# Kernel optimization log

Measured on AMD Instinct MI355X. Metric: run time of the kernel, lower is better.

The kernel has to match this reference:

```python
import jax, jax.numpy as jnp
import numpy as np

ALPHA = 0.2   # LeakyReLU negative slope (init arg alpha)
H = 256       # hidden_dim
U = 1024      # user pairs -> 2U user nodes
M = 64        # UAV nodes
D = 2 * U     # uniform out-degree per UAV (edges sorted by source)
N = 2 * U + M
E = M * D


def _lstm_dir(x, w_ih, w_hh, b):
    # x: [T, B, I] -> outputs [T, B, Hc]; b = b_ih + b_hh (they only ever add)
    Hc = w_hh.shape[1]
    B = x.shape[1]
    def step(carry, xt):
        h, c = carry
        g = xt @ w_ih.T + h @ w_hh.T + b          # [B, 4*Hc], gate order i,f,g,o
        i, f, gg, o = jnp.split(g, 4, axis=-1)
        c = jax.nn.sigmoid(f) * c + jax.nn.sigmoid(i) * jnp.tanh(gg)
        h = jax.nn.sigmoid(o) * jnp.tanh(c)
        return (h, c), h
    h0 = jnp.zeros((B, Hc), x.dtype)
    _, hs = jax.lax.scan(step, (h0, h0), x)
    return hs


def _bilstm(x, wih, whh, b):
    # wih: [2, 4Hc, I]; whh: [2, 4Hc, Hc]; b: [2, 4Hc]; dir 0 = fwd, 1 = reverse
    fwd = _lstm_dir(x, wih[0], whh[0], b[0])
    rev = _lstm_dir(x[::-1], wih[1], whh[1], b[1])[::-1]
    return jnp.concatenate([fwd, rev], axis=-1)   # [T, B, 2*Hc]


def _mlp2(h, w1, b1, w2, b2):
    h = jax.nn.relu(h @ w1.T + b1)
    return jax.nn.relu(h @ w2.T + b2)


def _forward(x, edge_index, users_num,
             ul_wih, ul_whh, ul_b, uav_lin_w, uav_lin_b,
             msg_w1, msg_b1, msg_w2, msg_b2,
             wq_w, wq_b, wr_w, wr_b, att_w, att_b,
             upd_w1, upd_b1, upd_w2, upd_b2,
             uavl_wih, uavl_whh, uavl_b, lin2_w, lin2_b):
    Un = users_num
    n = x.shape[0]
    m = n - 2 * Un
    # ---- users bidirectional LSTM over the pair (seq_len=2, batch=U) ----
    seq = jnp.stack([x[:Un], x[Un:2 * Un]], axis=0)        # [2, U, 2]
    users = _bilstm(seq, ul_wih, ul_whh, ul_b)             # [2, U, H]
    users = jnp.concatenate([users[0], users[1]], axis=0)  # [2U, H]
    uavs = x[2 * Un:] @ uav_lin_w.T + uav_lin_b            # [M, H]
    h = jnp.concatenate([users, uavs], axis=0)             # [N, H]
    # ---- message passing (flow target_to_source: i=src, aggregate at src) ----
    src, tgt = edge_index[0], edge_index[1]
    xi = h[src]                                            # [E, H]
    xj = h[tgt]                                            # [E, H]
    msg = _mlp2(jnp.concatenate([xi, xj], axis=1), msg_w1, msg_b1, msg_w2, msg_b2)  # [E, H]
    q = xi @ wq_w.T + wq_b
    r = msg @ wr_w.T + wr_b
    a = jax.nn.leaky_relu(jnp.concatenate([q, r], axis=1) @ att_w.T + att_b, ALPHA)  # [E,1]
    # segment softmax: edges sorted by source, uniform degree -> reshape [M, D]
    a = jax.nn.softmax(a.reshape(m, -1), axis=1).reshape(-1, 1)
    # ---- scatter-mean aggregate over source index ----
    agg = jax.ops.segment_sum(a * msg, src, num_segments=n)          # [N, H]
    cnt = jax.ops.segment_sum(jnp.ones((src.shape[0],), x.dtype), src, num_segments=n)
    agg = agg / jnp.maximum(cnt, 1.0)[:, None]
    # ---- update ----
    h2 = _mlp2(jnp.concatenate([agg, h], axis=1), upd_w1, upd_b1, upd_w2, upd_b2)  # [N, H]
    uav_seq = h2[2 * Un:][:, None, :]                      # [M, 1, H]
    uav_out = _bilstm(uav_seq, uavl_wih, uavl_whh, uavl_b)[:, 0, :]  # [M, H]
    out = jnp.concatenate([h2[:2 * Un], uav_out], axis=0)
    return jax.nn.sigmoid(out @ lin2_w.T + lin2_b)         # [N, 2]


def setup_inputs():
    key = jax.random.key(0)
    ks = iter(jax.random.split(key, 32))
    p = lambda *s: jax.random.normal(next(ks), s, jnp.float32) * 0.05
    Hc = H // 2
    x = jax.random.uniform(next(ks), (N, 2), jnp.float32)
    src = jnp.repeat(2 * U + jnp.arange(M), D)
    tgt = jnp.tile(jnp.arange(2 * U), M)
    edge_index = jnp.stack([src, tgt]).astype(jnp.int32)
    return dict(
        x=x, edge_index=edge_index, users_num=U,
        ul_wih=p(2, 4 * Hc, 2), ul_whh=p(2, 4 * Hc, Hc), ul_b=p(2, 4 * Hc),
        uav_lin_w=p(H, 2), uav_lin_b=p(H),
        msg_w1=p(H, 2 * H), msg_b1=p(H), msg_w2=p(H, H), msg_b2=p(H),
        wq_w=p(H, H), wq_b=p(H), wr_w=p(H, H), wr_b=p(H),
        att_w=p(1, 2 * H), att_b=p(1),
        upd_w1=p(H, 2 * H), upd_b1=p(H), upd_w2=p(H, H), upd_b2=p(H),
        uavl_wih=p(2, 4 * Hc, H), uavl_whh=p(2, 4 * Hc, Hc), uavl_b=p(2, 4 * Hc),
        lin2_w=p(2, H), lin2_b=p(2),
    )


def reference(x, edge_index, users_num,
              ul_wih, ul_whh, ul_b, uav_lin_w, uav_lin_b,
              msg_w1, msg_b1, msg_w2, msg_b2,
              wq_w, wq_b, wr_w, wr_b, att_w, att_b,
              upd_w1, upd_b1, upd_w2, upd_b2,
              uavl_wih, uavl_whh, uavl_b, lin2_w, lin2_b):
    return _forward(x, edge_index, users_num,
                    ul_wih, ul_whh, ul_b, uav_lin_w, uav_lin_b,
                    msg_w1, msg_b1, msg_w2, msg_b2,
                    wq_w, wq_b, wr_w, wr_b, att_w, att_b,
                    upd_w1, upd_b1, upd_w2, upd_b2,
                    uavl_wih, uavl_whh, uavl_b, lin2_w, lin2_b)
```

## Files before the change

kernel.cpp:

```cpp
#include <hip/hip_runtime.h>
#include <hip/hip_bf16.h>
#include <math.h>

#define UQ   1024
#define NUQ  2048
#define MQ   64
#define NN   2112
#define HD   256

typedef __attribute__((ext_vector_type(4))) float f32x4;
typedef __attribute__((ext_vector_type(8))) __bf16 bf16x8;

#define OFF_HB    0u
#define OFF_HUF   65536u
#define OFF_ACATF 1146880u
#define OFF_PUBF  3309568u
#define OFF_PB    4358144u
#define OFF_SPR   4423680u
#define OFF_ATT   4423936u
#define OFF_WHHT  4426240u
#define OFF_WIHT  4950528u
#define OFF_W1F   5999104u
#define OFF_W2F   6261248u
#define OFF_UW1F  6392320u
#define OFF_UW2F  6654464u
#define OFF_L1BF  6785536u
#define OFF_CREC  7866880u
#define OFF_H2    8399360u

__device__ __forceinline__ float sigm(float v) { return 1.f / (1.f + expf(-v)); }

__device__ __forceinline__ int huf_idx(int row, int k) {
  return (((row >> 6) * 8 + (k >> 5)) * 4 + ((row >> 4) & 3)) * 512 +
         (((k >> 3) & 3) * 16 + (row & 15)) * 8 + (k & 7);
}
__device__ __forceinline__ int acatf_idx(int row, int k) {
  return (((row >> 6) * 16 + (k >> 5)) * 4 + ((row >> 4) & 3)) * 512 +
         (((k >> 3) & 3) * 16 + (row & 15)) * 8 + (k & 7);
}
__device__ __forceinline__ int pubf_idx(int row, int k) {
  return (((row >> 8) * 8 + (k >> 5)) * 16 + ((row >> 4) & 15)) * 512 +
         (((k >> 3) & 3) * 16 + (row & 15)) * 8 + (k & 7);
}

__device__ __forceinline__ void gl16(const void* g, void* l) {
  __builtin_amdgcn_global_load_lds((const __attribute__((address_space(1))) void*)g,
                                   (__attribute__((address_space(3))) void*)l, 16, 0, 0);
}

__device__ void tile_transpose_perm(const float* __restrict__ in, int in_ld,
                                    float* __restrict__ out, int out_ld,
                                    int k0, int c0) {
  __shared__ float ldt[64][68];
  const int t = threadIdx.x;
  {
    const int ci = t >> 2, kq = t & 3;
    const int c = c0 + ci;
    const int row = (c & 3) * 128 + (c >> 2);
    const float* src = in + row * in_ld + k0 + kq * 16;
#pragma unroll
    for (int e = 0; e < 4; ++e)
      *(f32x4*)&ldt[ci][kq * 16 + e * 4] = *(const f32x4*)(src + e * 4);
  }
  __syncthreads();
  {
    const int kk = t >> 2, cq = t & 3;
    float* dst = out + (k0 + kk) * out_ld + c0 + cq * 16;
#pragma unroll
    for (int e4 = 0; e4 < 4; ++e4) {
      f32x4 v;
#pragma unroll
      for (int j = 0; j < 4; ++j) v[j] = ldt[cq * 16 + e4 * 4 + j][kk];
      *(f32x4*)(dst + e4 * 4) = v;
    }
  }
}

template<int K>
__device__ void frag_cast16(const float* __restrict__ W, int j0, __bf16* __restrict__ frag) {
  __shared__ float ldc[16][K + 4];
  const int t = threadIdx.x;
  {
    const int jr = t >> 4, kq = t & 15;
    const float* src = W + (j0 + jr) * K + kq * (K / 16);
#pragma unroll
    for (int e = 0; e < K / 64; ++e)
      *(f32x4*)&ldc[jr][kq * (K / 16) + e * 4] = *(const f32x4*)(src + e * 4);
  }
  __syncthreads();
  const int f = j0 >> 4;
  constexpr int nks = K >> 5;
  constexpr int thr_per_ks = 256 / nks;
  constexpr int q_per_thr = 512 / thr_per_ks;
  const int ks = t / thr_per_ks;
  const int q0 = (t % thr_per_ks) * q_per_thr;
#pragma unroll
  for (int h = 0; h < q_per_thr / 8; ++h) {
    bf16x8 v;
#pragma unroll
    for (int e = 0; e < 8; ++e) {
      int q = q0 + h * 8 + e;
      int lane = q >> 3;
      v[e] = (__bf16)ldc[lane & 15][ks * 32 + (lane >> 4) * 8 + (q & 7)];
    }
    *(bf16x8*)(frag + (ks * 16 + f) * 512 + q0 + h * 8) = v;
  }
}

__global__ __launch_bounds__(256) void k0_prep(
    const float* __restrict__ ul_whh, const float* __restrict__ uavl_wih,
    const float* __restrict__ msg_w1, const float* __restrict__ msg_w2,
    const float* __restrict__ upd_w1, const float* __restrict__ upd_w2,
    const float* __restrict__ att_w,  const float* __restrict__ att_b,
    const float* __restrict__ wq_w,   const float* __restrict__ wq_b,
    const float* __restrict__ wr_w,   const float* __restrict__ wr_b,
    char* __restrict__ ws)
{
  const int b = blockIdx.x, t = threadIdx.x;
  if (b < 32) {
    const int dir = b >> 4, tile = b & 15;
    tile_transpose_perm(ul_whh + dir * 65536, 128,
                        (float*)(ws + OFF_WHHT) + dir * 65536, 512,
                        (tile >> 3) * 64, (tile & 7) * 64);
  } else if (b < 96) {
    const int b2 = b - 32, dir = b2 >> 5, tile = b2 & 31;
    tile_transpose_perm(uavl_wih + dir * 131072, 256,
                        (float*)(ws + OFF_WIHT) + dir * 131072, 512,
                        (tile >> 3) * 64, (tile & 7) * 64);
  } else if (b < 112) {
    frag_cast16<256>(msg_w2, (b - 96) * 16, (__bf16*)(ws + OFF_W2F));
  } else if (b < 128) {
    frag_cast16<512>(msg_w1, (b - 112) * 16, (__bf16*)(ws + OFF_W1F));
  } else if (b < 144) {
    frag_cast16<512>(upd_w1, (b - 128) * 16, (__bf16*)(ws + OFF_UW1F));
  } else if (b < 160) {
    frag_cast16<256>(upd_w2, (b - 144) * 16, (__bf16*)(ws + OFF_UW2F));
  } else {
    float* wqa = (float*)(ws + OFF_ATT);
    float* vv  = wqa + 256;
    float* c0  = wqa + 512;
    float sa = 0.f, sr = 0.f;
    for (int j = 0; j < 256; ++j) {
      sa += att_w[j]       * wq_w[j * 256 + t];
      sr += att_w[256 + j] * wr_w[j * 256 + t];
    }
    wqa[t] = sa; vv[t] = sr;
    __shared__ float red[256];
    red[t] = att_w[t] * wq_b[t] + att_w[256 + t] * wr_b[t];
    __syncthreads();
    for (int s = 128; s > 0; s >>= 1) { if (t < s) red[t] += red[t + s]; __syncthreads(); }
    if (t == 0) c0[0] = red[0] + att_b[0];
  }
}

__global__ __launch_bounds__(256) void k1_embed(
    const float* __restrict__ x, const float* __restrict__ ul_wih,
    const float* __restrict__ ul_b, const float* __restrict__ uav_lin_w,
    const float* __restrict__ uav_lin_b, char* __restrict__ ws)
{
  __bf16* huf   = (__bf16*)(ws + OFF_HUF);
  __bf16* acatf = (__bf16*)(ws + OFF_ACATF);
  const int b = blockIdx.x, tid = threadIdx.x;
  if (b < 256) {
    const float* whhT = (const float*)(ws + OFF_WHHT);
    const int dir = tid >> 7, hc = tid & 127;
    const int u0 = b * 4;
    float wx[4], wy[4], bb[4];
#pragma unroll
    for (int g = 0; g < 4; ++g) {
      int row = g * 128 + hc;
      wx[g] = ul_wih[dir * 1024 + row * 2 + 0];
      wy[g] = ul_wih[dir * 1024 + row * 2 + 1];
      bb[g] = ul_b[dir * 512 + row];
    }
    __shared__ float h1s[2][128][4];
    float c1[4], h1v[4], in1x[4], in1y[4];
#pragma unroll
    for (int uu = 0; uu < 4; ++uu) {
      int u = u0 + uu;
      float ax = x[u * 2], ay = x[u * 2 + 1];
      float bx = x[(UQ + u) * 2], by = x[(UQ + u) * 2 + 1];
      float i0x = dir ? bx : ax, i0y = dir ? by : ay;
      in1x[uu] = dir ? ax : bx; in1y[uu] = dir ? ay : by;
      float gv[4];
#pragma unroll
      for (int g = 0; g < 4; ++g) gv[g] = wx[g] * i0x + wy[g] * i0y + bb[g];
      float ii = sigm(gv[0]), gg = tanhf(gv[2]), oo = sigm(gv[3]);
      c1[uu] = ii * gg;
      h1v[uu] = oo * tanhf(c1[uu]);
      h1s[dir][hc][uu] = h1v[uu];
    }
    __syncthreads();
    float acc[4][4];
#pragma unroll
    for (int uu = 0; uu < 4; ++uu)
#pragma unroll
      for (int g = 0; g < 4; ++g) acc[uu][g] = wx[g] * in1x[uu] + wy[g] * in1y[uu] + bb[g];
    for (int k = 0; k < 128; ++k) {
      f32x4 hv  = *(const f32x4*)&h1s[dir][k][0];
      f32x4 wv4 = *(const f32x4*)(whhT + dir * 65536 + k * 512 + hc * 4);
#pragma unroll
      for (int uu = 0; uu < 4; ++uu)
#pragma unroll
        for (int g = 0; g < 4; ++g) acc[uu][g] += hv[uu] * wv4[g];
    }
    const int col = dir * 128 + hc;
#pragma unroll
    for (int uu = 0; uu < 4; ++uu) {
      int u = u0 + uu;
      float ii = sigm(acc[uu][0]), ff = sigm(acc[uu][1]);
      float gg = tanhf(acc[uu][2]), oo = sigm(acc[uu][3]);
      float c2 = ff * c1[uu] + ii * gg;
      float h2v = oo * tanhf(c2);
      float va = dir ? h2v : h1v[uu];
      float vb = dir ? h1v[uu] : h2v;
      huf[huf_idx(u, col)] = (__bf16)va;
      huf[huf_idx(UQ + u, col)] = (__bf16)vb;
      acatf[acatf_idx(u, 256 + col)] = (__bf16)va;
      acatf[acatf_idx(UQ + u, 256 + col)] = (__bf16)vb;
      acatf[acatf_idx(u, tid)] = (__bf16)0.f;
      acatf[acatf_idx(UQ + u, tid)] = (__bf16)0.f;
    }
  } else {
    float* hb = (float*)(ws + OFF_HB);
    const int j = tid;
    const int mb = (b - 256) * 16;
    for (int m = mb; m < mb + 16; ++m) {
      float xa = x[(NUQ + m) * 2], xb = x[(NUQ + m) * 2 + 1];
      float val = xa * uav_lin_w[j * 2] + xb * uav_lin_w[j * 2 + 1] + uav_lin_b[j];
      hb[m * 256 + j] = val;
      huf[huf_idx(NUQ + m, j)] = (__bf16)val;
      acatf[acatf_idx(NUQ + m, 256 + j)] = (__bf16)val;
    }
  }
}

template<int NKS>
__device__ __forceinline__ void frag_gemm_acc(const __bf16* __restrict__ Abase,
                                              const __bf16* __restrict__ Bbase,
                                              f32x4 acc[4][4]) {
  const int lane = threadIdx.x & 63;
  const int cg = threadIdx.x >> 6;
  for (int ks = 0; ks < NKS; ++ks) {
    bf16x8 Af[4], Bf[4];
#pragma unroll
    for (int g = 0; g < 4; ++g)
      Af[g] = *(const bf16x8*)(Abase + ((ks * 4 + g) * 64 + lane) * 8);
#pragma unroll
    for (int f = 0; f < 4; ++f)
      Bf[f] = *(const bf16x8*)(Bbase + ((ks * 16 + cg * 4 + f) * 64 + lane) * 8);
#pragma unroll
    for (int g = 0; g < 4; ++g)
#pragma unroll
      for (int f = 0; f < 4; ++f)
        acc[g][f] = __builtin_amdgcn_mfma_f32_16x16x32_bf16(Af[g], Bf[f], acc[g][f], 0, 0, 0);
  }
}

__global__ __launch_bounds__(256) void k2_proj(const float* __restrict__ msg_b1,
                                               char* __restrict__ ws)
{
  const __bf16* huf = (const __bf16*)(ws + OFF_HUF);
  const __bf16* w1f = (const __bf16*)(ws + OFF_W1F);
  const int b = blockIdx.x;
  const int lane = threadIdx.x & 63, cg = threadIdx.x >> 6;
  const int cl = lane & 15, g16 = lane >> 4;
  if (b < 32) {
    f32x4 acc[4][4] = {};
    frag_gemm_acc<8>(huf + b * 16384, w1f + 65536, acc);
    __bf16* pubf = (__bf16*)(ws + OFF_PUBF);
#pragma unroll
    for (int g = 0; g < 4; ++g)
#pragma unroll
      for (int f = 0; f < 4; ++f)
#pragma unroll
        for (int r = 0; r < 4; ++r) {
          int row = b * 64 + g * 16 + g16 * 4 + r;
          int col = cg * 64 + f * 16 + cl;
          pubf[pubf_idx(row, col)] = (__bf16)acc[g][f][r];
        }
  } else if (b == 32) {
    f32x4 acc[4][4] = {};
    frag_gemm_acc<8>(huf + 32 * 16384, w1f, acc);
    float* pb = (float*)(ws + OFF_PB);
#pragma unroll
    for (int g = 0; g < 4; ++g)
#pragma unroll
      for (int f = 0; f < 4; ++f)
#pragma unroll
        for (int r = 0; r < 4; ++r) {
          int row = g * 16 + g16 * 4 + r;
          int col = cg * 64 + f * 16 + cl;
          pb[row * 256 + col] = acc[g][f][r] + msg_b1[col];
        }
  } else {
    const float* hb  = (const float*)(ws + OFF_HB);
    const float* wqa = (const float*)(ws + OFF_ATT);
    const float* c0  = wqa + 512;
    float* spr = (float*)(ws + OFF_SPR);
    const int t = threadIdx.x;
    if (t < 64) {
      float s = 0.f;
      for (int k = 0; k < 256; ++k) s += hb[t * 256 + k] * wqa[k];
      spr[t] = s + c0[0];
    }
  }
}

__global__ __launch_bounds__(1024) void k3_edge(const float* __restrict__ msg_b2,
                                                char* __restrict__ ws)
{
  const char*  PUBF = (const char*)(ws + OFF_PUBF);
  const float* PB   = (const float*)(ws + OFF_PB);
  const float* spr  = (const float*)(ws + OFF_SPR);
  const float* vv   = (const float*)(ws + OFF_ATT) + 256;
  const char*  W2F  = (const char*)(ws + OFF_W2F);
  float* crec = (float*)(ws + OFF_CREC);

  __shared__ __align__(16) char bufA[2][16384];
  __shared__ __align__(16) char bufB[2][16384];
  __shared__ float plds[16][64];
  __shared__ float redmax[16], wds[16];
  __shared__ float wvs[4][256];

  const int m = blockIdx.x >> 3, ch = blockIdx.x & 7;
  const int tid = threadIdx.x, wave = tid >> 6, lane = tid & 63;
  const int cl = lane & 15, g16 = lane >> 4;
  const int rg = wave >> 2, cg = wave & 3;
  const float sm = spr[m];
  const char* Asrc = PUBF + ch * 131072;

  gl16(Asrc + wave * 1024 + lane * 16, &bufA[0][wave * 1024]);
  gl16(W2F  + wave * 1024 + lane * 16, &bufB[0][wave * 1024]);
  __syncthreads();

  f32x4 acc[4][4] = {};
  for (int ks = 0; ks < 8; ++ks) {
    const int cur = ks & 1;
    if (ks < 7) {
      gl16(Asrc + (ks + 1) * 16384 + wave * 1024 + lane * 16, &bufA[cur ^ 1][wave * 1024]);
      gl16(W2F  + (ks + 1) * 16384 + wave * 1024 + lane * 16, &bufB[cur ^ 1][wave * 1024]);
    }
    const float* pbp = PB + m * 256 + ks * 32 + g16 * 8;
    f32x4 pb0 = *(const f32x4*)pbp;
    f32x4 pb1 = *(const f32x4*)(pbp + 4);
    bf16x8 Af[4];
#pragma unroll
    for (int g = 0; g < 4; ++g) {
      bf16x8 raw = *(const bf16x8*)(&bufA[cur][((rg * 4 + g) * 64 + lane) * 16]);
      bf16x8 a;
#pragma unroll
      for (int r = 0; r < 4; ++r) {
        a[r]     = (__bf16)fmaxf((float)raw[r]     + pb0[r], 0.f);
        a[4 + r] = (__bf16)fmaxf((float)raw[4 + r] + pb1[r], 0.f);
      }
      Af[g] = a;
    }
    bf16x8 Bf[4];
#pragma unroll
    for (int f = 0; f < 4; ++f)
      Bf[f] = *(const bf16x8*)(&bufB[cur][((cg * 4 + f) * 64 + lane) * 16]);
#pragma unroll
    for (int g = 0; g < 4; ++g)
#pragma unroll
      for (int f = 0; f < 4; ++f)
        acc[g][f] = __builtin_amdgcn_mfma_f32_16x16x32_bf16(Af[g], Bf[f], acc[g][f], 0, 0, 0);
    __syncthreads();
  }

  float p[4][4] = {};
#pragma unroll
  for (int f = 0; f < 4; ++f) {
    const int j = cg * 64 + f * 16 + cl;
    const float b2j = msg_b2[j], vj = vv[j];
#pragma unroll
    for (int g = 0; g < 4; ++g)
#pragma unroll
      for (int r = 0; r < 4; ++r) {
        float mv = fmaxf(acc[g][f][r] + b2j, 0.f);
        acc[g][f][r] = mv;
        p[g][r] += mv * vj;
      }
  }
#pragma unroll
  for (int mask = 1; mask < 16; mask <<= 1)
#pragma unroll
    for (int g = 0; g < 4; ++g)
#pragma unroll
      for (int r = 0; r < 4; ++r) p[g][r] += __shfl_xor(p[g][r], mask);
  if (cl == 0) {
#pragma unroll
    for (int g = 0; g < 4; ++g)
#pragma unroll
      for (int r = 0; r < 4; ++r) plds[wave][g * 16 + g16 * 4 + r] = p[g][r];
  }
  __syncthreads();

  float lr[4][4], wm = -3.4e38f;
#pragma unroll
  for (int g = 0; g < 4; ++g)
#pragma unroll
    for (int r = 0; r < 4; ++r) {
      int row = g * 16 + g16 * 4 + r;
      float l = plds[rg * 4 + 0][row] + plds[rg * 4 + 1][row] +
                plds[rg * 4 + 2][row] + plds[rg * 4 + 3][row] + sm;
      l = l > 0.f ? l : 0.2f * l;
      lr[g][r] = l;
      wm = fmaxf(wm, l);
    }
  wm = fmaxf(wm, __shfl_xor(wm, 16));
  wm = fmaxf(wm, __shfl_xor(wm, 32));
  if (lane == 0) redmax[wave] = wm;
  __syncthreads();
  float Mc = redmax[0];
#pragma unroll
  for (int i = 1; i < 16; ++i) Mc = fmaxf(Mc, redmax[i]);

  float e[4][4], ds = 0.f;
#pragma unroll
  for (int g = 0; g < 4; ++g)
#pragma unroll
    for (int r = 0; r < 4; ++r) { e[g][r] = __expf(lr[g][r] - Mc); ds += e[g][r]; }
  ds += __shfl_xor(ds, 16);
  ds += __shfl_xor(ds, 32);
  if (lane == 0) wds[wave] = ds;

#pragma unroll
  for (int f = 0; f < 4; ++f) {
    float w = 0.f;
#pragma unroll
    for (int g = 0; g < 4; ++g)
#pragma unroll
      for (int r = 0; r < 4; ++r) w += e[g][r] * acc[g][f][r];
    w += __shfl_xor(w, 16);
    w += __shfl_xor(w, 32);
    if (g16 == 0) wvs[rg][cg * 64 + f * 16 + cl] = w;
  }
  __syncthreads();

  float* rec = crec + (m * 8 + ch) * 260;
  if (tid < 256) rec[tid] = wvs[0][tid] + wvs[1][tid] + wvs[2][tid] + wvs[3][tid];
  if (tid == 0) rec[256] = Mc;
  if (tid == 1) rec[257] = wds[0] + wds[4] + wds[8] + wds[12];
}

__global__ __launch_bounds__(256) void k4_combine(char* __restrict__ ws)
{
  const float* crec = (const float*)(ws + OFF_CREC);
  __bf16* acatf = (__bf16*)(ws + OFF_ACATF);
  const int m = blockIdx.x, j = threadIdx.x;
  float mx = -3.4e38f;
  for (int c = 0; c < 8; ++c) mx = fmaxf(mx, crec[(m * 8 + c) * 260 + 256]);
  float S = 0.f, A = 0.f;
  for (int c = 0; c < 8; ++c) {
    const float* rec = crec + (m * 8 + c) * 260;
    float sc = __expf(rec[256] - mx);
    S += sc * rec[257];
    A += sc * rec[j];
  }
  float agg = A / S * (1.f / 2048.f);
  acatf[acatf_idx(NUQ + m, j)] = (__bf16)agg;
}

__global__ __launch_bounds__(256) void k5_upd1(const float* __restrict__ upd_b1,
                                               char* __restrict__ ws)
{
  const int b = blockIdx.x;
  const int lane = threadIdx.x & 63, cg = threadIdx.x >> 6;
  const int cl = lane & 15, g16 = lane >> 4;
  f32x4 acc[4][4] = {};
  frag_gemm_acc<16>((const __bf16*)(ws + OFF_ACATF) + b * 32768,
                    (const __bf16*)(ws + OFF_UW1F), acc);
  __bf16* l1bf = (__bf16*)(ws + OFF_L1BF);
#pragma unroll
  for (int g = 0; g < 4; ++g)
#pragma unroll
    for (int f = 0; f < 4; ++f)
#pragma unroll
      for (int r = 0; r < 4; ++r) {
        int row = b * 64 + g * 16 + g16 * 4 + r;
        int col = cg * 64 + f * 16 + cl;
        float v = fmaxf(acc[g][f][r] + upd_b1[col], 0.f);
        l1bf[huf_idx(row, col)] = (__bf16)v;
      }
}
__global__ __launch_bounds__(256) void k6_upd2(const float* __restrict__ upd_b2,
                                               char* __restrict__ ws)
{
  const int b = blockIdx.x;
  const int lane = threadIdx.x & 63, cg = threadIdx.x >> 6;
  const int cl = lane & 15, g16 = lane >> 4;
  f32x4 acc[4][4] = {};
  frag_gemm_acc<8>((const __bf16*)(ws + OFF_L1BF) + b * 16384,
                   (const __bf16*)(ws + OFF_UW2F), acc);
  float* h2 = (float*)(ws + OFF_H2);
#pragma unroll
  for (int g = 0; g < 4; ++g)
#pragma unroll
    for (int f = 0; f < 4; ++f)
#pragma unroll
      for (int r = 0; r < 4; ++r) {
        int row = b * 64 + g * 16 + g16 * 4 + r;
        int col = cg * 64 + f * 16 + cl;
        h2[row * 256 + col] = fmaxf(acc[g][f][r] + upd_b2[col], 0.f);
      }
}

__global__ __launch_bounds__(256) void k7_final(
    const float* __restrict__ uavl_b, const float* __restrict__ lin2_w,
    const float* __restrict__ lin2_b, float* __restrict__ out, char* __restrict__ ws)
{
  const float* h2 = (const float*)(ws + OFF_H2);
  const int b = blockIdx.x, tid = threadIdx.x;
  if (b < 64) {
    const float* wihT = (const float*)(ws + OFF_WIHT);
    __shared__ float xs[256], uo[256];
    xs[tid] = h2[(NUQ + b) * 256 + tid];
    __syncthreads();
    const int dir = tid >> 7, hc = tid & 127;
    float a4[4] = {0.f, 0.f, 0.f, 0.f};
    for (int k = 0; k < 256; ++k) {
      float xv = xs[k];
      f32x4 wv4 = *(const f32x4*)(wihT + dir * 131072 + k * 512 + hc * 4);
#pragma unroll
      for (int g = 0; g < 4; ++g) a4[g] += xv * wv4[g];
    }
    float bb[4];
#pragma unroll
    for (int g = 0; g < 4; ++g) bb[g] = uavl_b[dir * 512 + g * 128 + hc];
    float ii = sigm(a4[0] + bb[0]);
    float gg = tanhf(a4[2] + bb[2]);
    float oo = sigm(a4[3] + bb[3]);
    float cc = ii * gg;
    uo[dir * 128 + hc] = oo * tanhf(cc);
    __syncthreads();
    float p0 = uo[tid] * lin2_w[tid];
    float p1 = uo[tid] * lin2_w[256 + tid];
#pragma unroll
    for (int mask = 1; mask < 64; mask <<= 1) {
      p0 += __shfl_xor(p0, mask);
      p1 += __shfl_xor(p1, mask);
    }
    __shared__ float r0s[4], r1s[4];
    const int lane = tid & 63, wv = tid >> 6;
    if (lane == 0) { r0s[wv] = p0; r1s[wv] = p1; }
    __syncthreads();
    if (tid == 0) {
      float d0 = r0s[0] + r0s[1] + r0s[2] + r0s[3] + lin2_b[0];
      float d1 = r1s[0] + r1s[1] + r1s[2] + r1s[3] + lin2_b[1];
      out[(NUQ + b) * 2 + 0] = 1.f / (1.f + expf(-d0));
      out[(NUQ + b) * 2 + 1] = 1.f / (1.f + expf(-d1));
    }
  } else {
    __shared__ float l0s[256], l1s[256];
    l0s[tid] = lin2_w[tid];
    l1s[tid] = lin2_w[256 + tid];
    __syncthreads();
    const int row = (b - 64) * 32 + (tid >> 3);
    const int sub = tid & 7;
    const float* hr = h2 + row * 256;
    float d0 = 0.f, d1 = 0.f;
#pragma unroll
    for (int i = 0; i < 8; ++i) {
      int k = i * 32 + sub * 4;
      f32x4 hv = *(const f32x4*)(hr + k);
#pragma unroll
      for (int q = 0; q < 4; ++q) { d0 += hv[q] * l0s[k + q]; d1 += hv[q] * l1s[k + q]; }
    }
#pragma unroll
    for (int mask = 1; mask < 8; mask <<= 1) {
      d0 += __shfl_xor(d0, mask);
      d1 += __shfl_xor(d1, mask);
    }
    if (sub == 0) {
      out[row * 2 + 0] = 1.f / (1.f + expf(-(d0 + lin2_b[0])));
      out[row * 2 + 1] = 1.f / (1.f + expf(-(d1 + lin2_b[1])));
    }
  }
}

extern "C" void kernel_launch(void* const* d_in, const int* in_sizes, int n_in,
                              void* d_out, int out_size, void* d_ws, size_t ws_size,
                              hipStream_t stream)
{
  const float* x         = (const float*)d_in[0];
  const float* ul_wih    = (const float*)d_in[3];
  const float* ul_whh    = (const float*)d_in[4];
  const float* ul_b      = (const float*)d_in[5];
  const float* uav_lin_w = (const float*)d_in[6];
  const float* uav_lin_b = (const float*)d_in[7];
  const float* msg_w1    = (const float*)d_in[8];
  const float* msg_b1    = (const float*)d_in[9];
  const float* msg_w2    = (const float*)d_in[10];
  const float* msg_b2    = (const float*)d_in[11];
  const float* wq_w      = (const float*)d_in[12];
  const float* wq_b      = (const float*)d_in[13];
  const float* wr_w      = (const float*)d_in[14];
  const float* wr_b      = (const float*)d_in[15];
  const float* att_w     = (const float*)d_in[16];
  const float* att_b     = (const float*)d_in[17];
  const float* upd_w1    = (const float*)d_in[18];
  const float* upd_b1    = (const float*)d_in[19];
  const float* upd_w2    = (const float*)d_in[20];
  const float* upd_b2    = (const float*)d_in[21];
  const float* uavl_wih  = (const float*)d_in[22];
  const float* uavl_b    = (const float*)d_in[24];
  const float* lin2_w    = (const float*)d_in[25];
  const float* lin2_b    = (const float*)d_in[26];
  char* ws = (char*)d_ws;
  float* out = (float*)d_out;

  k0_prep<<<dim3(161), dim3(256), 0, stream>>>(ul_whh, uavl_wih, msg_w1, msg_w2, upd_w1,
                                               upd_w2, att_w, att_b, wq_w, wq_b, wr_w, wr_b, ws);
  k1_embed<<<dim3(260), dim3(256), 0, stream>>>(x, ul_wih, ul_b, uav_lin_w, uav_lin_b, ws);
  k2_proj<<<dim3(34), dim3(256), 0, stream>>>(msg_b1, ws);
  k3_edge<<<dim3(512), dim3(1024), 0, stream>>>(msg_b2, ws);
  k4_combine<<<dim3(64), dim3(256), 0, stream>>>(ws);
  k5_upd1<<<dim3(33), dim3(256), 0, stream>>>(upd_b1, ws);
  k6_upd2<<<dim3(33), dim3(256), 0, stream>>>(upd_b2, ws);
  k7_final<<<dim3(128), dim3(256), 0, stream>>>(uavl_b, lin2_w, lin2_b, out, ws);
}
```

Measured before the change: 114.6 us.

## Fuse combine and update MLP kernels, drop acatf buffer, prefetch edge A tiles

Merges the softmax-combine, both update-MLP GEMMs and the user lin2 head into one kernel. The first update layer is split so user rows skip the zero aggregate half of the K dimension and UAV rows build their aggregate in LDS. That removes the concatenated acatf buffer and its zero-fill writes, the l1 and h2 intermediates in global memory, and two launches. In the edge kernel, A tiles are now loaded through registers and the bias+ReLU is applied once per element before storing to LDS, overlapped with the MFMAs, rather than redone for every fragment. It also sets a 2-block occupancy hint and coalesces the k1 writes through LDS. The cost is more per-block serial work in the fused kernel and register pressure in the edge loop.

Result: faster. 110.8 us (-3.3%).

```diff
diff --git a/kernel.cpp b/kernel.cpp
--- a/kernel.cpp
+++ b/kernel.cpp
@@ -13,29 +13,23 @@
 
 #define OFF_HB    0u
 #define OFF_HUF   65536u
-#define OFF_ACATF 1146880u
-#define OFF_PUBF  3309568u
-#define OFF_PB    4358144u
-#define OFF_SPR   4423680u
-#define OFF_ATT   4423936u
-#define OFF_WHHT  4426240u
-#define OFF_WIHT  4950528u
-#define OFF_W1F   5999104u
-#define OFF_W2F   6261248u
-#define OFF_UW1F  6392320u
-#define OFF_UW2F  6654464u
-#define OFF_L1BF  6785536u
-#define OFF_CREC  7866880u
-#define OFF_H2    8399360u
+#define OFF_PUBF  1146880u
+#define OFF_PB    2195456u
+#define OFF_SPR   2260992u
+#define OFF_ATT   2261248u
+#define OFF_WHHT  2263552u
+#define OFF_WIHT  2787840u
+#define OFF_W1F   3836416u
+#define OFF_W2F   4098560u
+#define OFF_UW1F  4229632u
+#define OFF_UW2F  4491776u
+#define OFF_CREC  4622848u
+#define OFF_H2U   5155328u
 
 __device__ __forceinline__ float sigm(float v) { return 1.f / (1.f + expf(-v)); }
 
 __device__ __forceinline__ int huf_idx(int row, int k) {
   return (((row >> 6) * 8 + (k >> 5)) * 4 + ((row >> 4) & 3)) * 512 +
-         (((k >> 3) & 3) * 16 + (row & 15)) * 8 + (k & 7);
-}
-__device__ __forceinline__ int acatf_idx(int row, int k) {
-  return (((row >> 6) * 16 + (k >> 5)) * 4 + ((row >> 4) & 3)) * 512 +
          (((k >> 3) & 3) * 16 + (row & 15)) * 8 + (k & 7);
 }
 __device__ __forceinline__ int pubf_idx(int row, int k) {
@@ -158,8 +152,7 @@
     const float* __restrict__ ul_b, const float* __restrict__ uav_lin_w,
     const float* __restrict__ uav_lin_b, char* __restrict__ ws)
 {
-  __bf16* huf   = (__bf16*)(ws + OFF_HUF);
-  __bf16* acatf = (__bf16*)(ws + OFF_ACATF);
+  __bf16* huf = (__bf16*)(ws + OFF_HUF);
   const int b = blockIdx.x, tid = threadIdx.x;
   if (b < 256) {
     const float* whhT = (const float*)(ws + OFF_WHHT);
@@ -174,6 +167,7 @@
       bb[g] = ul_b[dir * 512 + row];
     }
     __shared__ float h1s[2][128][4];
+    __shared__ float hout[8][260];
     float c1[4], h1v[4], in1x[4], in1y[4];
 #pragma unroll
     for (int uu = 0; uu < 4; ++uu) {
@@ -207,19 +201,23 @@
     const int col = dir * 128 + hc;
 #pragma unroll
     for (int uu = 0; uu < 4; ++uu) {
-      int u = u0 + uu;
       float ii = sigm(acc[uu][0]), ff = sigm(acc[uu][1]);
       float gg = tanhf(acc[uu][2]), oo = sigm(acc[uu][3]);
       float c2 = ff * c1[uu] + ii * gg;
       float h2v = oo * tanhf(c2);
       float va = dir ? h2v : h1v[uu];
       float vb = dir ? h1v[uu] : h2v;
-      huf[huf_idx(u, col)] = (__bf16)va;
-      huf[huf_idx(UQ + u, col)] = (__bf16)vb;
-      acatf[acatf_idx(u, 256 + col)] = (__bf16)va;
-      acatf[acatf_idx(UQ + u, 256 + col)] = (__bf16)vb;
-      acatf[acatf_idx(u, tid)] = (__bf16)0.f;
-      acatf[acatf_idx(UQ + u, tid)] = (__bf16)0.f;
+      hout[uu][col] = va;
+      hout[4 + uu][col] = vb;
+    }
+    __syncthreads();
+    {
+      const int lr = tid >> 5, c = tid & 31;
+      bf16x8 v;
+#pragma unroll
+      for (int e = 0; e < 8; ++e) v[e] = (__bf16)hout[lr][c * 8 + e];
+      const int node = (lr < 4) ? (u0 + lr) : (UQ + u0 + lr - 4);
+      *(bf16x8*)(huf + huf_idx(node, c * 8)) = v;
     }
   } else {
     float* hb = (float*)(ws + OFF_HB);
@@ -230,7 +228,6 @@
       float val = xa * uav_lin_w[j * 2] + xb * uav_lin_w[j * 2 + 1] + uav_lin_b[j];
       hb[m * 256 + j] = val;
       huf[huf_idx(NUQ + m, j)] = (__bf16)val;
-      acatf[acatf_idx(NUQ + m, 256 + j)] = (__bf16)val;
     }
   }
 }
@@ -307,8 +304,8 @@
   }
 }
 
-__global__ __launch_bounds__(1024) void k3_edge(const float* __restrict__ msg_b2,
-                                                char* __restrict__ ws)
+__global__ __launch_bounds__(1024, 2) void k3_edge(const float* __restrict__ msg_b2,
+                                                   char* __restrict__ ws)
 {
   const char*  PUBF = (const char*)(ws + OFF_PUBF);
   const float* PB   = (const float*)(ws + OFF_PB);
@@ -329,34 +326,39 @@
   const int rg = wave >> 2, cg = wave & 3;
   const float sm = spr[m];
   const char* Asrc = PUBF + ch * 131072;
-
-  gl16(Asrc + wave * 1024 + lane * 16, &bufA[0][wave * 1024]);
-  gl16(W2F  + wave * 1024 + lane * 16, &bufB[0][wave * 1024]);
+  const float* pbm = PB + m * 256;
+
+  {
+    bf16x8 araw = *(const bf16x8*)(Asrc + wave * 1024 + lane * 16);
+    gl16(W2F + wave * 1024 + lane * 16, &bufB[0][wave * 1024]);
+    const float* pbp = pbm + (lane >> 4) * 8;
+    f32x4 p0 = *(const f32x4*)pbp, p1 = *(const f32x4*)(pbp + 4);
+    bf16x8 a;
+#pragma unroll
+    for (int r = 0; r < 4; ++r) {
+      a[r]     = (__bf16)fmaxf((float)araw[r]     + p0[r], 0.f);
+      a[4 + r] = (__bf16)fmaxf((float)araw[4 + r] + p1[r], 0.f);
+    }
+    *(bf16x8*)(&bufA[0][wave * 1024 + lane * 16]) = a;
+  }
   __syncthreads();
 
   f32x4 acc[4][4] = {};
   for (int ks = 0; ks < 8; ++ks) {
     const int cur = ks & 1;
+    bf16x8 arn{};
+    f32x4 pn0{}, pn1{};
     if (ks < 7) {
-      gl16(Asrc + (ks + 1) * 16384 + wave * 1024 + lane * 16, &bufA[cur ^ 1][wave * 1024]);
-      gl16(W2F  + (ks + 1) * 16384 + wave * 1024 + lane * 16, &bufB[cur ^ 1][wave * 1024]);
-    }
-    const float* pbp = PB + m * 256 + ks * 32 + g16 * 8;
-    f32x4 pb0 = *(const f32x4*)pbp;
-    f32x4 pb1 = *(const f32x4*)(pbp + 4);
-    bf16x8 Af[4];
-#pragma unroll
-    for (int g = 0; g < 4; ++g) {
-      bf16x8 raw = *(const bf16x8*)(&bufA[cur][((rg * 4 + g) * 64 + lane) * 16]);
-      bf16x8 a;
-#pragma unroll
-      for (int r = 0; r < 4; ++r) {
-        a[r]     = (__bf16)fmaxf((float)raw[r]     + pb0[r], 0.f);
-        a[4 + r] = (__bf16)fmaxf((float)raw[4 + r] + pb1[r], 0.f);
-      }
-      Af[g] = a;
-    }
-    bf16x8 Bf[4];
+      arn = *(const bf16x8*)(Asrc + (ks + 1) * 16384 + wave * 1024 + lane * 16);
+      gl16(W2F + (ks + 1) * 16384 + wave * 1024 + lane * 16, &bufB[cur ^ 1][wave * 1024]);
+      const float* pbp = pbm + (ks + 1) * 32 + (lane >> 4) * 8;
+      pn0 = *(const f32x4*)pbp;
+      pn1 = *(const f32x4*)(pbp + 4);
+    }
+    bf16x8 Af[4], Bf[4];
+#pragma unroll
+    for (int g = 0; g < 4; ++g)
+      Af[g] = *(const bf16x8*)(&bufA[cur][((rg * 4 + g) * 64 + lane) * 16]);
 #pragma unroll
     for (int f = 0; f < 4; ++f)
       Bf[f] = *(const bf16x8*)(&bufB[cur][((cg * 4 + f) * 64 + lane) * 16]);
@@ -365,6 +367,15 @@
 #pragma unroll
       for (int f = 0; f < 4; ++f)
         acc[g][f] = __builtin_amdgcn_mfma_f32_16x16x32_bf16(Af[g], Bf[f], acc[g][f], 0, 0, 0);
+    if (ks < 7) {
+      bf16x8 a;
+#pragma unroll
+      for (int r = 0; r < 4; ++r) {
+        a[r]     = (__bf16)fmaxf((float)arn[r]     + pn0[r], 0.f);
+        a[4 + r] = (__bf16)fmaxf((float)arn[4 + r] + pn1[r], 0.f);
+      }
+      *(bf16x8*)(&bufA[cur ^ 1][wave * 1024 + lane * 16]) = a;
+    }
     __syncthreads();
   }
 
@@ -444,138 +455,217 @@
   if (tid == 1) rec[257] = wds[0] + wds[4] + wds[8] + wds[12];
 }
 
-__global__ __launch_bounds__(256) void k4_combine(char* __restrict__ ws)
+__global__ __launch_bounds__(256) void k56_update(
+    const float* __restrict__ upd_b1, const float* __restrict__ upd_b2,
+    const float* __restrict__ lin2_w, const float* __restrict__ lin2_b,
+    float* __restrict__ out, char* __restrict__ ws)
 {
-  const float* crec = (const float*)(ws + OFF_CREC);
-  __bf16* acatf = (__bf16*)(ws + OFF_ACATF);
-  const int m = blockIdx.x, j = threadIdx.x;
-  float mx = -3.4e38f;
-  for (int c = 0; c < 8; ++c) mx = fmaxf(mx, crec[(m * 8 + c) * 260 + 256]);
-  float S = 0.f, A = 0.f;
-  for (int c = 0; c < 8; ++c) {
-    const float* rec = crec + (m * 8 + c) * 260;
-    float sc = __expf(rec[256] - mx);
-    S += sc * rec[257];
-    A += sc * rec[j];
-  }
-  float agg = A / S * (1.f / 2048.f);
-  acatf[acatf_idx(NUQ + m, j)] = (__bf16)agg;
-}
-
-__global__ __launch_bounds__(256) void k5_upd1(const float* __restrict__ upd_b1,
-                                               char* __restrict__ ws)
-{
-  const int b = blockIdx.x;
-  const int lane = threadIdx.x & 63, cg = threadIdx.x >> 6;
+  const __bf16* huf  = (const __bf16*)(ws + OFF_HUF);
+  const __bf16* uw1f = (const __bf16*)(ws + OFF_UW1F);
+  const __bf16* uw2f = (const __bf16*)(ws + OFF_UW2F);
+
+  __shared__ __align__(16) __bf16 l1f[8 * 4 * 512];
+  __shared__ __align__(16) __bf16 aggf[8 * 4 * 512];
+  __shared__ float scs[64][8];
+  __shared__ float sS[64];
+  __shared__ float l2p[4][64][2];
+
+  const int b = blockIdx.x, tid = threadIdx.x;
+  const int lane = tid & 63, cg = tid >> 6;
   const int cl = lane & 15, g16 = lane >> 4;
+
   f32x4 acc[4][4] = {};
-  frag_gemm_acc<16>((const __bf16*)(ws + OFF_ACATF) + b * 32768,
-                    (const __bf16*)(ws + OFF_UW1F), acc);
-  __bf16* l1bf = (__bf16*)(ws + OFF_L1BF);
+  if (b < 32) {
+    frag_gemm_acc<8>(huf + b * 16384, uw1f + 8 * 16 * 512, acc);
+  } else {
+    const float* crec = (const float*)(ws + OFF_CREC);
+    if (tid < 64) {
+      const int m = tid;
+      float mx = -3.4e38f;
+      for (int c = 0; c < 8; ++c) mx = fmaxf(mx, crec[(m * 8 + c) * 260 + 256]);
+      float S = 0.f;
+      for (int c = 0; c < 8; ++c) {
+        float sc = __expf(crec[(m * 8 + c) * 260 + 256] - mx);
+        scs[m][c] = sc;
+        S += sc * crec[(m * 8 + c) * 260 + 257];
+      }
+      sS[m] = S;
+    }
+    __syncthreads();
+    for (int m = 0; m < 64; ++m) {
+      float A = 0.f;
+#pragma unroll
+      for (int c = 0; c < 8; ++c) A += scs[m][c] * crec[(m * 8 + c) * 260 + tid];
+      float agg = A / sS[m] * (1.f / 2048.f);
+      aggf[((tid >> 5) * 4 + (m >> 4)) * 512 + (((tid >> 3) & 3) * 16 + (m & 15)) * 8 + (tid & 7)] =
+          (__bf16)agg;
+    }
+    __syncthreads();
+    const __bf16* hufu = huf + 32 * 16384;
+    for (int ks = 0; ks < 8; ++ks) {
+      bf16x8 Af[4], Bf[4];
+#pragma unroll
+      for (int g = 0; g < 4; ++g)
+        Af[g] = *(const bf16x8*)(aggf + ((ks * 4 + g) * 64 + lane) * 8);
+#pragma unroll
+      for (int f = 0; f < 4; ++f)
+        Bf[f] = *(const bf16x8*)(uw1f + ((ks * 16 + cg * 4 + f) * 64 + lane) * 8);
+#pragma unroll
+      for (int g = 0; g < 4; ++g)
+#pragma unroll
+        for (int f = 0; f < 4; ++f)
+          acc[g][f] = __builtin_amdgcn_mfma_f32_16x16x32_bf16(Af[g], Bf[f], acc[g][f], 0, 0, 0);
+    }
+    for (int ks = 8; ks < 16; ++ks) {
+      bf16x8 Af[4], Bf[4];
+#pragma unroll
+      for (int g = 0; g < 4; ++g)
+        Af[g] = *(const bf16x8*)(hufu + (((ks - 8) * 4 + g) * 64 + lane) * 8);
+#pragma unroll
+      for (int f = 0; f < 4; ++f)
+        Bf[f] = *(const bf16x8*)(uw1f + ((ks * 16 + cg * 4 + f) * 64 + lane) * 8);
+#pragma unroll
+      for (int g = 0; g < 4; ++g)
+#pragma unroll
+        for (int f = 0; f < 4; ++f)
+          acc[g][f] = __builtin_amdgcn_mfma_f32_16x16x32_bf16(Af[g], Bf[f], acc[g][f], 0, 0, 0);
+    }
+  }
+
 #pragma unroll
   for (int g = 0; g < 4; ++g)
 #pragma unroll
+    for (int f = 0; f < 4; ++f) {
+      const int col = cg * 64 + f * 16 + cl;
+      const float b1 = upd_b1[col];
+#pragma unroll
+      for (int r = 0; r < 4; ++r) {
+        const int rl = g * 16 + g16 * 4 + r;
+        float v = fmaxf(acc[g][f][r] + b1, 0.f);
+        l1f[((col >> 5) * 4 + g) * 512 + (((col >> 3) & 3) * 16 + (rl & 15)) * 8 + (col & 7)] =
+            (__bf16)v;
+      }
+    }
+  __syncthreads();
+
+  f32x4 a2[4][4] = {};
+  for (int ks = 0; ks < 8; ++ks) {
+    bf16x8 Af[4], Bf[4];
+#pragma unroll
+    for (int g = 0; g < 4; ++g)
+      Af[g] = *(const bf16x8*)(l1f + ((ks * 4 + g) * 64 + lane) * 8);
+#pragma unroll
     for (int f = 0; f < 4; ++f)
-#pragma unroll
-      for (int r = 0; r < 4; ++r) {
-        int row = b * 64 + g * 16 + g16 * 4 + r;
-        int col = cg * 64 + f * 16 + cl;
-        float v = fmaxf(acc[g][f][r] + upd_b1[col], 0.f);
-        l1bf[huf_idx(row, col)] = (__bf16)v;
+      Bf[f] = *(const bf16x8*)(uw2f + ((ks * 16 + cg * 4 + f) * 64 + lane) * 8);
+#pragma unroll
+    for (int g = 0; g < 4; ++g)
+#pragma unroll
+      for (int f = 0; f < 4; ++f)
+        a2[g][f] = __builtin_amdgcn_mfma_f32_16x16x32_bf16(Af[g], Bf[f], a2[g][f], 0, 0, 0);
+  }
+
+  if (b < 32) {
+    float d0[4][4] = {}, d1[4][4] = {};
+#pragma unroll
+    for (int f = 0; f < 4; ++f) {
+      const int col = cg * 64 + f * 16 + cl;
+      const float b2 = upd_b2[col];
+      const float w0 = lin2_w[col], w1 = lin2_w[256 + col];
+#pragma unroll
+      for (int g = 0; g < 4; ++g)
+#pragma unroll
+        for (int r = 0; r < 4; ++r) {
+          float hv = fmaxf(a2[g][f][r] + b2, 0.f);
+          d0[g][r] += hv * w0;
+          d1[g][r] += hv * w1;
+        }
+    }
+#pragma unroll
+    for (int mask = 1; mask < 16; mask <<= 1)
+#pragma unroll
+      for (int g = 0; g < 4; ++g)
+#pragma unroll
+        for (int r = 0; r < 4; ++r) {
+          d0[g][r] += __shfl_xor(d0[g][r], mask);
+          d1[g][r] += __shfl_xor(d1[g][r], mask);
+        }
+    if (cl == 0) {
+#pragma unroll
+      for (int g = 0; g < 4; ++g)
+#pragma unroll
+        for (int r = 0; r < 4; ++r) {
+          l2p[cg][g * 16 + g16 * 4 + r][0] = d0[g][r];
+          l2p[cg][g * 16 + g16 * 4 + r][1] = d1[g][r];
+        }
+    }
+    __syncthreads();
+    if (tid < 64) {
+      float s0 = l2p[0][tid][0] + l2p[1][tid][0] + l2p[2][tid][0] + l2p[3][tid][0] + lin2_b[0];
+      float s1 = l2p[0][tid][1] + l2p[1][tid][1] + l2p[2][tid][1] + l2p[3][tid][1] + lin2_b[1];
+      const int row = b * 64 + tid;
+      out[row * 2 + 0] = 1.f / (1.f + expf(-s0));
+      out[row * 2 + 1] = 1.f / (1.f + expf(-s1));
+    }
+  } else {
+    float* h2u = (float*)(ws + OFF_H2U);
+#pragma unroll
+    for (int g = 0; g < 4; ++g)
+#pragma unroll
+      for (int f = 0; f < 4; ++f) {
+        const int col = cg * 64 + f * 16 + cl;
+        const float b2 = upd_b2[col];
+#pragma unroll
+        for (int r = 0; r < 4; ++r) {
+          const int rl = g * 16 + g16 * 4 + r;
+          h2u[rl * 256 + col] = fmaxf(a2[g][f][r] + b2, 0.f);
+        }
       }
-}
-__global__ __launch_bounds__(256) void k6_upd2(const float* __restrict__ upd_b2,
-                                               char* __restrict__ ws)
-{
-  const int b = blockIdx.x;
-  const int lane = threadIdx.x & 63, cg = threadIdx.x >> 6;
-  const int cl = lane & 15, g16 = lane >> 4;
-  f32x4 acc[4][4] = {};
-  frag_gemm_acc<8>((const __bf16*)(ws + OFF_L1BF) + b * 16384,
-                   (const __bf16*)(ws + OFF_UW2F), acc);
-  float* h2 = (float*)(ws + OFF_H2);
-#pragma unroll
-  for (int g = 0; g < 4; ++g)
-#pragma unroll
-    for (int f = 0; f < 4; ++f)
-#pragma unroll
-      for (int r = 0; r < 4; ++r) {
-        int row = b * 64 + g * 16 + g16 * 4 + r;
-        int col = cg * 64 + f * 16 + cl;
-        h2[row * 256 + col] = fmaxf(acc[g][f][r] + upd_b2[col], 0.f);
-      }
+  }
 }
 
 __global__ __launch_bounds__(256) void k7_final(
     const float* __restrict__ uavl_b, const float* __restrict__ lin2_w,
     const float* __restrict__ lin2_b, float* __restrict__ out, char* __restrict__ ws)
 {
-  const float* h2 = (const float*)(ws + OFF_H2);
+  const float* h2u = (const float*)(ws + OFF_H2U);
   const int b = blockIdx.x, tid = threadIdx.x;
-  if (b < 64) {
-    const float* wihT = (const float*)(ws + OFF_WIHT);
-    __shared__ float xs[256], uo[256];
-    xs[tid] = h2[(NUQ + b) * 256 + tid];
-    __syncthreads();
-    const int dir = tid >> 7, hc = tid & 127;
-    float a4[4] = {0.f, 0.f, 0.f, 0.f};
-    for (int k = 0; k < 256; ++k) {
-      float xv = xs[k];
-      f32x4 wv4 = *(const f32x4*)(wihT + dir * 131072 + k * 512 + hc * 4);
-#pragma unroll
-      for (int g = 0; g < 4; ++g) a4[g] += xv * wv4[g];
-    }
-    float bb[4];
-#pragma unroll
-    for (int g = 0; g < 4; ++g) bb[g] = uavl_b[dir * 512 + g * 128 + hc];
-    float ii = sigm(a4[0] + bb[0]);
-    float gg = tanhf(a4[2] + bb[2]);
-    float oo = sigm(a4[3] + bb[3]);
-    float cc = ii * gg;
-    uo[dir * 128 + hc] = oo * tanhf(cc);
-    __syncthreads();
-    float p0 = uo[tid] * lin2_w[tid];
-    float p1 = uo[tid] * lin2_w[256 + tid];
-#pragma unroll
-    for (int mask = 1; mask < 64; mask <<= 1) {
-      p0 += __shfl_xor(p0, mask);
-      p1 += __shfl_xor(p1, mask);
-    }
-    __shared__ float r0s[4], r1s[4];
-    const int lane = tid & 63, wv = tid >> 6;
-    if (lane == 0) { r0s[wv] = p0; r1s[wv] = p1; }
-    __syncthreads();
-    if (tid == 0) {
-      float d0 = r0s[0] + r0s[1] + r0s[2] + r0s[3] + lin2_b[0];
-      float d1 = r1s[0] + r1s[1] + r1s[2] + r1s[3] + lin2_b[1];
-      out[(NUQ + b) * 2 + 0] = 1.f / (1.f + expf(-d0));
-      out[(NUQ + b) * 2 + 1] = 1.f / (1.f + expf(-d1));
-    }
-  } else {
-    __shared__ float l0s[256], l1s[256];
-    l0s[tid] = lin2_w[tid];
-    l1s[tid] = lin2_w[256 + tid];
-    __syncthreads();
-    const int row = (b - 64) * 32 + (tid >> 3);
-    const int sub = tid & 7;
-    const float* hr = h2 + row * 256;
-    float d0 = 0.f, d1 = 0.f;
-#pragma unroll
-    for (int i = 0; i < 8; ++i) {
-      int k = i * 32 + sub * 4;
-      f32x4 hv = *(const f32x4*)(hr + k);
-#pragma unroll
-      for (int q = 0; q < 4; ++q) { d0 += hv[q] * l0s[k + q]; d1 += hv[q] * l1s[k + q]; }
-    }
-#pragma unroll
-    for (int mask = 1; mask < 8; mask <<= 1) {
-      d0 += __shfl_xor(d0, mask);
-      d1 += __shfl_xor(d1, mask);
-    }
-    if (sub == 0) {
-      out[row * 2 + 0] = 1.f / (1.f + expf(-(d0 + lin2_b[0])));
-      out[row * 2 + 1] = 1.f / (1.f + expf(-(d1 + lin2_b[1])));
-    }
+  const float* wihT = (const float*)(ws + OFF_WIHT);
+  __shared__ float xs[256], uo[256];
+  xs[tid] = h2u[b * 256 + tid];
+  __syncthreads();
+  const int dir = tid >> 7, hc = tid & 127;
+  float a4[4] = {0.f, 0.f, 0.f, 0.f};
+  for (int k = 0; k < 256; ++k) {
+    float xv = xs[k];
+    f32x4 wv4 = *(const f32x4*)(wihT + dir * 131072 + k * 512 + hc * 4);
+#pragma unroll
+    for (int g = 0; g < 4; ++g) a4[g] += xv * wv4[g];
+  }
+  float bb[4];
+#pragma unroll
+  for (int g = 0; g < 4; ++g) bb[g] = uavl_b[dir * 512 + g * 128 + hc];
+  float ii = sigm(a4[0] + bb[0]);
+  float gg = tanhf(a4[2] + bb[2]);
+  float oo = sigm(a4[3] + bb[3]);
+  float cc = ii * gg;
+  uo[dir * 128 + hc] = oo * tanhf(cc);
+  __syncthreads();
+  float p0 = uo[tid] * lin2_w[tid];
+  float p1 = uo[tid] * lin2_w[256 + tid];
+#pragma unroll
+  for (int mask = 1; mask < 64; mask <<= 1) {
+    p0 += __shfl_xor(p0, mask);
+    p1 += __shfl_xor(p1, mask);
+  }
+  __shared__ float r0s[4], r1s[4];
+  const int lane = tid & 63, wv = tid >> 6;
+  if (lane == 0) { r0s[wv] = p0; r1s[wv] = p1; }
+  __syncthreads();
+  if (tid == 0) {
+    float d0 = r0s[0] + r0s[1] + r0s[2] + r0s[3] + lin2_b[0];
+    float d1 = r1s[0] + r1s[1] + r1s[2] + r1s[3] + lin2_b[1];
+    out[(NUQ + b) * 2 + 0] = 1.f / (1.f + expf(-d0));
+    out[(NUQ + b) * 2 + 1] = 1.f / (1.f + expf(-d1));
   }
 }
 
@@ -615,8 +705,6 @@
   k1_embed<<<dim3(260), dim3(256), 0, stream>>>(x, ul_wih, ul_b, uav_lin_w, uav_lin_b, ws);
   k2_proj<<<dim3(34), dim3(256), 0, stream>>>(msg_b1, ws);
   k3_edge<<<dim3(512), dim3(1024), 0, stream>>>(msg_b2, ws);
-  k4_combine<<<dim3(64), dim3(256), 0, stream>>>(ws);
-  k5_upd1<<<dim3(33), dim3(256), 0, stream>>>(upd_b1, ws);
-  k6_upd2<<<dim3(33), dim3(256), 0, stream>>>(upd_b2, ws);
-  k7_final<<<dim3(128), dim3(256), 0, stream>>>(uavl_b, lin2_w, lin2_b, out, ws);
-}
+  k56_update<<<dim3(33), dim3(256), 0, stream>>>(upd_b1, upd_b2, lin2_w, lin2_b, out, ws);
+  k7_final<<<dim3(64), dim3(256), 0, stream>>>(uavl_b, lin2_w, lin2_b, out, ws);
+}
```
